# Performance work log

Measured on AMD Instinct MI355X. Metric: run time of the kernel, lower is better.

## Reference

```python
import jax, jax.numpy as jnp
import numpy as np

B, C_IN, C_OUT, H, W, K = 64, 64, 128, 64, 64, 3


def setup_inputs() -> dict:
    key = jax.random.key(0)
    k1, k2, k3 = jax.random.split(key, 3)
    x = jax.random.normal(k1, (B, C_IN, H, W), dtype=jnp.float32)
    weight = jax.random.normal(k2, (C_OUT, C_IN, K, K), dtype=jnp.float32)
    bias = jax.random.normal(k3, (C_OUT, 1, 1), dtype=jnp.float32)
    return {"x": x, "weight": weight, "bias": bias}


def reference(x, weight, bias):
    # Valid (no pad), stride-1, NCHW direct conv + broadcast bias, matching
    # the naive nested-loop conv2d_multi_in_out + bias of MyConv2D.
    out = jax.lax.conv_general_dilated(
        x, weight,
        window_strides=(1, 1),
        padding="VALID",
        dimension_numbers=("NCHW", "OIHW", "NCHW"),
    )
    return out + bias  # bias (C_out,1,1) broadcasts over (B, C_out, H_out, W_out)
```

## Files before the change

kernel.cpp:

```cpp
#include <hip/hip_runtime.h>

#define CI 64
#define CO 128
#define HH 64
#define WW 64
#define OH 62
#define OW 62

typedef __attribute__((ext_vector_type(8))) short short8x;
typedef __attribute__((ext_vector_type(16))) float f32x16;

__device__ __forceinline__ ushort bf16rne(float f) {
    unsigned u = __builtin_bit_cast(unsigned, f);
    u += 0x7fffu + ((u >> 16) & 1u);
    return (ushort)(u >> 16);
}

__global__ __launch_bounds__(256)
void wprep(const float* __restrict__ w, ushort* __restrict__ wt) {
    const int idx = blockIdx.x * 256 + threadIdx.x;
    const int kk = idx >> 13;
    const int rem = idx & 8191;
    const int co = rem >> 6, ci = rem & 63;
    wt[idx] = bf16rne(w[(co * 64 + ci) * 9 + kk]);
}

__global__ __launch_bounds__(256, 2)
void conv_fused(const float* __restrict__ x, const ushort* __restrict__ wt,
                const float* __restrict__ bias, float* __restrict__ out) {
    __shared__ ushort Xl[264 * 64];
    __shared__ float  sB[128];

    const int tid = threadIdx.x;
    const int wv = tid >> 6, L = tid & 63, l31 = L & 31, q = L >> 5;
    const int b = blockIdx.y, oh0 = blockIdx.x * 2;
    const int m0 = (wv >> 1) * 64;
    const int rw = wv & 1;

    if (tid < 128) sB[tid] = bias[tid];

    for (int pxi = tid; pxi < 264; pxi += 256) {
        const int r = pxi / 66, cpos = pxi - r * 66;
        const int ih = oh0 + r;
        const bool valid = cpos < 64;
        const float* xcol = x + (((size_t)b * CI) * HH + ih) * WW + cpos;
        ushort* dst = &Xl[pxi * 64];
        const int pm = pxi & 7;
        #pragma unroll
        for (int c = 0; c < 8; ++c) {
            ushort tmp[8];
            #pragma unroll
            for (int j = 0; j < 8; ++j) {
                float v = valid ? xcol[(c * 8 + j) * (HH * WW)] : 0.f;
                tmp[j] = bf16rne(v);
            }
            *(uint4*)(dst + ((c ^ pm) * 8)) = *(const uint4*)tmp;
        }
    }

    short8x wbuf[2][8];
    const ushort* wbase = wt + (m0 + l31) * 64 + q * 8;
    #pragma unroll
    for (int h = 0; h < 2; ++h)
        #pragma unroll
        for (int s = 0; s < 4; ++s)
            wbuf[0][h * 4 + s] = *(const short8x*)(wbase + h * 2048 + s * 16);

    f32x16 acc[2][2];
    #pragma unroll
    for (int i = 0; i < 2; ++i)
        #pragma unroll
        for (int j = 0; j < 2; ++j)
            #pragma unroll
            for (int r = 0; r < 16; ++r) acc[i][j][r] = 0.f;

    __syncthreads();

    #pragma unroll
    for (int kk = 0; kk < 9; ++kk) {
        const short8x* wf = wbuf[kk & 1];
        if (kk < 8) {
            const ushort* nb = wbase + (kk + 1) * 8192;
            #pragma unroll
            for (int h = 0; h < 2; ++h)
                #pragma unroll
                for (int s = 0; s < 4; ++s)
                    wbuf[(kk + 1) & 1][h * 4 + s] = *(const short8x*)(nb + h * 2048 + s * 16);
        }
        const int kr = kk / 3, kc = kk - kr * 3;
        const int pxb = (rw + kr) * 66 + kc + l31;
        const ushort* bb0 = Xl + pxb * 64;
        const int f0 = pxb & 7;
        #pragma unroll
        for (int s = 0; s < 4; ++s) {
            const int cch = s * 2 + q;
            short8x b0 = *(const short8x*)(bb0 + ((cch ^ f0) * 8));
            short8x b1 = *(const short8x*)(bb0 + 32 * 64 + ((cch ^ f0) * 8));
            acc[0][0] = __builtin_amdgcn_mfma_f32_32x32x16_bf16(wf[s],     b0, acc[0][0], 0, 0, 0);
            acc[0][1] = __builtin_amdgcn_mfma_f32_32x32x16_bf16(wf[s],     b1, acc[0][1], 0, 0, 0);
            acc[1][0] = __builtin_amdgcn_mfma_f32_32x32x16_bf16(wf[4 + s], b0, acc[1][0], 0, 0, 0);
            acc[1][1] = __builtin_amdgcn_mfma_f32_32x32x16_bf16(wf[4 + s], b1, acc[1][1], 0, 0, 0);
        }
    }

    const int oh = oh0 + rw;
    #pragma unroll
    for (int ti = 0; ti < 2; ++ti)
        #pragma unroll
        for (int tj = 0; tj < 2; ++tj) {
            const int col = tj * 32 + l31;
            if (col < OW) {
                #pragma unroll
                for (int reg = 0; reg < 16; ++reg) {
                    const int co = m0 + ti * 32 + 4 * q + (reg & 3) + 8 * (reg >> 2);
                    out[(((size_t)b * CO + co) * OH + oh) * OW + col] = acc[ti][tj][reg] + sB[co];
                }
            }
        }
}

extern "C" void kernel_launch(void* const* d_in, const int* in_sizes, int n_in,
                              void* d_out, int out_size, void* d_ws, size_t ws_size,
                              hipStream_t stream) {
    const float* x    = (const float*)d_in[0];
    const float* wgt  = (const float*)d_in[1];
    const float* bias = (const float*)d_in[2];
    float* out = (float*)d_out;

    ushort* wt = (ushort*)d_ws;

    wprep<<<dim3(288), 256, 0, stream>>>(wgt, wt);
    conv_fused<<<dim3(31, 64), 256, 0, stream>>>(x, wt, bias, out);
}
```

Before: 255.5 us.

## Process eight output rows per block with rolling LDS ring and register prefetch

Each 512-thread block now walks eight output rows in pairs, keeping a four-row ring of bf16 input rows in LDS and prefetching the next two input rows into registers while the MFMAs run. The aim is to cut redundant input staging (each row was loaded by several blocks) and overlap global loads with compute. Weights now come straight from a device-global buffer per tap, with no double-buffered registers, and each wave covers 32 output channels instead of 64. The costs are fewer blocks (512), extra barriers per step, and weight reloads from cache on every tap.

```diff
diff --git a/kernel.cpp b/kernel.cpp
--- a/kernel.cpp
+++ b/kernel.cpp
@@ -10,6 +10,8 @@
 typedef __attribute__((ext_vector_type(8))) short short8x;
 typedef __attribute__((ext_vector_type(16))) float f32x16;
 
+__device__ ushort g_wt[9 * CO * CI];
+
 __device__ __forceinline__ ushort bf16rne(float f) {
     unsigned u = __builtin_bit_cast(unsigned, f);
     u += 0x7fffu + ((u >> 16) & 1u);
@@ -17,37 +19,40 @@
 }
 
 __global__ __launch_bounds__(256)
-void wprep(const float* __restrict__ w, ushort* __restrict__ wt) {
+void wprep(const float* __restrict__ w) {
     const int idx = blockIdx.x * 256 + threadIdx.x;
     const int kk = idx >> 13;
     const int rem = idx & 8191;
     const int co = rem >> 6, ci = rem & 63;
-    wt[idx] = bf16rne(w[(co * 64 + ci) * 9 + kk]);
+    g_wt[idx] = bf16rne(w[(co * 64 + ci) * 9 + kk]);
 }
 
-__global__ __launch_bounds__(256, 2)
-void conv_fused(const float* __restrict__ x, const ushort* __restrict__ wt,
-                const float* __restrict__ bias, float* __restrict__ out) {
+__global__ __launch_bounds__(512, 4)
+void conv_fused(const float* __restrict__ x, const float* __restrict__ bias,
+                float* __restrict__ out) {
     __shared__ ushort Xl[264 * 64];
-    __shared__ float  sB[128];
+    __shared__ float  sB[CO];
 
     const int tid = threadIdx.x;
     const int wv = tid >> 6, L = tid & 63, l31 = L & 31, q = L >> 5;
-    const int b = blockIdx.y, oh0 = blockIdx.x * 2;
-    const int m0 = (wv >> 1) * 64;
+    const int hq = wv >> 1;
     const int rw = wv & 1;
+    const int b = blockIdx.y, base = blockIdx.x * 8;
 
-    if (tid < 128) sB[tid] = bias[tid];
+    if (tid < CO) sB[tid] = bias[tid];
 
-    for (int pxi = tid; pxi < 264; pxi += 256) {
+    const float* xb = x + (size_t)b * CI * HH * WW;
+
+    for (int i = tid; i < 528; i += 512) {
+        const int pxi = i >> 1, half = i & 1;
         const int r = pxi / 66, cpos = pxi - r * 66;
-        const int ih = oh0 + r;
         const bool valid = cpos < 64;
-        const float* xcol = x + (((size_t)b * CI) * HH + ih) * WW + cpos;
+        const float* xcol = xb + (size_t)(base + r) * WW + cpos;
         ushort* dst = &Xl[pxi * 64];
         const int pm = pxi & 7;
         #pragma unroll
-        for (int c = 0; c < 8; ++c) {
+        for (int cc = 0; cc < 4; ++cc) {
+            const int c = half * 4 + cc;
             ushort tmp[8];
             #pragma unroll
             for (int j = 0; j < 8; ++j) {
@@ -58,65 +63,90 @@
         }
     }
 
-    short8x wbuf[2][8];
-    const ushort* wbase = wt + (m0 + l31) * 64 + q * 8;
+    const ushort* wbase = g_wt + (hq * 32 + l31) * 64 + q * 8;
+
+    f32x16 acc[2];
     #pragma unroll
-    for (int h = 0; h < 2; ++h)
+    for (int nt = 0; nt < 2; ++nt)
         #pragma unroll
-        for (int s = 0; s < 4; ++s)
-            wbuf[0][h * 4 + s] = *(const short8x*)(wbase + h * 2048 + s * 16);
+        for (int r = 0; r < 16; ++r) acc[nt][r] = 0.f;
 
-    f32x16 acc[2][2];
-    #pragma unroll
-    for (int i = 0; i < 2; ++i)
-        #pragma unroll
-        for (int j = 0; j < 2; ++j)
-            #pragma unroll
-            for (int r = 0; r < 16; ++r) acc[i][j][r] = 0.f;
+    const int pcol = tid & 63, prn = (tid >> 6) & 1, pcq = (tid >> 7) & 3;
 
     __syncthreads();
 
-    #pragma unroll
-    for (int kk = 0; kk < 9; ++kk) {
-        const short8x* wf = wbuf[kk & 1];
-        if (kk < 8) {
-            const ushort* nb = wbase + (kk + 1) * 8192;
+    for (int t = 0; t < 4; ++t) {
+        if (base + 2 * t >= OH) break;
+        const bool pf = (t < 3) && (base + 2 * t + 2 < OH);
+
+        float pv[2][8];
+        if (pf) {
+            const float* xc = xb + (size_t)(base + 2 * t + 4 + prn) * WW + pcol;
             #pragma unroll
-            for (int h = 0; h < 2; ++h)
+            for (int c = 0; c < 2; ++c)
                 #pragma unroll
-                for (int s = 0; s < 4; ++s)
-                    wbuf[(kk + 1) & 1][h * 4 + s] = *(const short8x*)(nb + h * 2048 + s * 16);
+                for (int j = 0; j < 8; ++j)
+                    pv[c][j] = xc[((pcq * 2 + c) * 8 + j) * (HH * WW)];
         }
-        const int kr = kk / 3, kc = kk - kr * 3;
-        const int pxb = (rw + kr) * 66 + kc + l31;
-        const ushort* bb0 = Xl + pxb * 64;
-        const int f0 = pxb & 7;
+
         #pragma unroll
-        for (int s = 0; s < 4; ++s) {
-            const int cch = s * 2 + q;
-            short8x b0 = *(const short8x*)(bb0 + ((cch ^ f0) * 8));
-            short8x b1 = *(const short8x*)(bb0 + 32 * 64 + ((cch ^ f0) * 8));
-            acc[0][0] = __builtin_amdgcn_mfma_f32_32x32x16_bf16(wf[s],     b0, acc[0][0], 0, 0, 0);
-            acc[0][1] = __builtin_amdgcn_mfma_f32_32x32x16_bf16(wf[s],     b1, acc[0][1], 0, 0, 0);
-            acc[1][0] = __builtin_amdgcn_mfma_f32_32x32x16_bf16(wf[4 + s], b0, acc[1][0], 0, 0, 0);
-            acc[1][1] = __builtin_amdgcn_mfma_f32_32x32x16_bf16(wf[4 + s], b1, acc[1][1], 0, 0, 0);
+        for (int kk = 0; kk < 9; ++kk) {
+            const int kr = kk / 3, kc = kk - kr * 3;
+            const int slot = (2 * t + rw + kr) & 3;
+            const int pxB0 = slot * 66 + kc + l31;
+            const ushort* bb = Xl + pxB0 * 64;
+            const int f = pxB0 & 7;
+            const ushort* wt_tap = wbase + kk * (CO * CI);
+            #pragma unroll
+            for (int s = 0; s < 4; ++s) {
+                short8x a  = *(const short8x*)(wt_tap + s * 16);
+                const int ob = (((s * 2 + q) ^ f) * 8);
+                short8x b0 = *(const short8x*)(bb + ob);
+                short8x b1 = *(const short8x*)(bb + 32 * 64 + ob);
+                acc[0] = __builtin_amdgcn_mfma_f32_32x32x16_bf16(a, b0, acc[0], 0, 0, 0);
+                acc[1] = __builtin_amdgcn_mfma_f32_32x32x16_bf16(a, b1, acc[1], 0, 0, 0);
+            }
+        }
+
+        {
+            const int oh = base + 2 * t + rw;
+            #pragma unroll
+            for (int nt = 0; nt < 2; ++nt) {
+                const int col = nt * 32 + l31;
+                if (col < OW) {
+                    #pragma unroll
+                    for (int reg = 0; reg < 16; ++reg) {
+                        const int co = hq * 32 + 4 * q + (reg & 3) + 8 * (reg >> 2);
+                        out[(((size_t)b * CO + co) * OH + oh) * OW + col] = acc[nt][reg] + sB[co];
+                    }
+                }
+                #pragma unroll
+                for (int r = 0; r < 16; ++r) acc[nt][r] = 0.f;
+            }
+        }
+
+        if (pf) {
+            __syncthreads();
+            const int slotn = (2 * t + prn) & 3;
+            const int pxn = slotn * 66 + pcol;
+            const int pmn = pxn & 7;
+            ushort* dst = &Xl[pxn * 64];
+            #pragma unroll
+            for (int c = 0; c < 2; ++c) {
+                ushort tmp[8];
+                #pragma unroll
+                for (int j = 0; j < 8; ++j) tmp[j] = bf16rne(pv[c][j]);
+                *(uint4*)(dst + (((pcq * 2 + c) ^ pmn) * 8)) = *(const uint4*)tmp;
+            }
+            if (tid < 32) {
+                const int zr = (tid >> 4) & 1, zc = 64 + ((tid >> 3) & 1), zch = tid & 7;
+                const int pxz = ((2 * t + zr) & 3) * 66 + zc;
+                const uint4 zz = {0u, 0u, 0u, 0u};
+                *(uint4*)(&Xl[pxz * 64 + ((zch ^ (pxz & 7)) * 8)]) = zz;
+            }
+            __syncthreads();
         }
     }
-
-    const int oh = oh0 + rw;
-    #pragma unroll
-    for (int ti = 0; ti < 2; ++ti)
-        #pragma unroll
-        for (int tj = 0; tj < 2; ++tj) {
-            const int col = tj * 32 + l31;
-            if (col < OW) {
-                #pragma unroll
-                for (int reg = 0; reg < 16; ++reg) {
-                    const int co = m0 + ti * 32 + 4 * q + (reg & 3) + 8 * (reg >> 2);
-                    out[(((size_t)b * CO + co) * OH + oh) * OW + col] = acc[ti][tj][reg] + sB[co];
-                }
-            }
-        }
 }
 
 extern "C" void kernel_launch(void* const* d_in, const int* in_sizes, int n_in,
@@ -127,8 +157,6 @@
     const float* bias = (const float*)d_in[2];
     float* out = (float*)d_out;
 
-    ushort* wt = (ushort*)d_ws;
-
-    wprep<<<dim3(288), 256, 0, stream>>>(wgt, wt);
-    conv_fused<<<dim3(31, 64), 256, 0, stream>>>(x, wt, bias, out);
+    wprep<<<dim3(288), 256, 0, stream>>>(wgt);
+    conv_fused<<<dim3(8, 64), 512, 0, stream>>>(x, bias, out);
 }
```

New measurement: 321.7 us. 1.26x slower.
